# Kernel tuning notes

Hardware: AMD Instinct MI355X
Metric: run time of the kernel (lower is better)

## Reference

```python
import jax, jax.numpy as jnp
import numpy as np

DIM = 768
HEADS = 12
HD = DIM // HEADS
B, NX, NY = 8, 1024, 1024
GRID = 32
FREQ = 100.0
MLP_HID = 4 * DIM
EPS = 1e-5


def _grid_pos(batch, n, grid):
    g = int(np.sqrt(n))
    yy, xx = jnp.meshgrid(jnp.arange(g, dtype=jnp.int32), jnp.arange(g, dtype=jnp.int32), indexing='ij')
    pos = jnp.stack([yy.reshape(-1), xx.reshape(-1)], axis=-1)  # [N,2]
    return jnp.broadcast_to(pos[None], (batch, n, 2))


def setup_inputs() -> dict:
    key = jax.random.key(0)
    ks = jax.random.split(key, 16)
    s = 0.02
    inp = {
        'x': jax.random.normal(ks[0], (B, NX, DIM), jnp.float32),
        'y': jax.random.normal(ks[1], (B, NY, DIM), jnp.float32),
        'xpos': _grid_pos(B, NX, GRID),
        'ypos': _grid_pos(B, NY, GRID),
        # norms (gamma, beta)
        'norm1_g': jnp.ones((DIM,), jnp.float32), 'norm1_b': jnp.zeros((DIM,), jnp.float32),
        'norm2_g': jnp.ones((DIM,), jnp.float32), 'norm2_b': jnp.zeros((DIM,), jnp.float32),
        'norm3_g': jnp.ones((DIM,), jnp.float32), 'norm3_b': jnp.zeros((DIM,), jnp.float32),
        'normy_g': jnp.ones((DIM,), jnp.float32), 'normy_b': jnp.zeros((DIM,), jnp.float32),
        # self-attn: fused qkv (no bias, qkv_bias=False), out proj (with bias)
        'qkv_w': jax.random.normal(ks[2], (DIM, 3 * DIM), jnp.float32) * s,
        'attn_proj_w': jax.random.normal(ks[3], (DIM, DIM), jnp.float32) * s,
        'attn_proj_b': jnp.zeros((DIM,), jnp.float32),
        # cross-attn: separate q/k/v (no bias), out proj (with bias)
        'projq_w': jax.random.normal(ks[4], (DIM, DIM), jnp.float32) * s,
        'projk_w': jax.random.normal(ks[5], (DIM, DIM), jnp.float32) * s,
        'projv_w': jax.random.normal(ks[6], (DIM, DIM), jnp.float32) * s,
        'cross_proj_w': jax.random.normal(ks[7], (DIM, DIM), jnp.float32) * s,
        'cross_proj_b': jnp.zeros((DIM,), jnp.float32),
        # MLP
        'fc1_w': jax.random.normal(ks[8], (DIM, MLP_HID), jnp.float32) * s,
        'fc1_b': jnp.zeros((MLP_HID,), jnp.float32),
        'fc2_w': jax.random.normal(ks[9], (MLP_HID, DIM), jnp.float32) * s,
        'fc2_b': jnp.zeros((DIM,), jnp.float32),
    }
    return inp


def layernorm(x, g, b):
    m = jnp.mean(x, axis=-1, keepdims=True)
    v = jnp.mean(jnp.square(x - m), axis=-1, keepdims=True)
    return (x - m) * jax.lax.rsqrt(v + EPS) * g + b


def rope1d(tok, pos):
    # tok: [B,H,N,D], pos: [B,N] int
    D = tok.shape[-1]
    inv = 1.0 / (FREQ ** (jnp.arange(0, D, 2, dtype=jnp.float32) / D))  # [D/2]
    f = pos[:, None, :, None].astype(jnp.float32) * inv  # [B,1,N,D/2]
    emb = jnp.concatenate([f, f], axis=-1)  # [B,1,N,D]
    cos, sin = jnp.cos(emb), jnp.sin(emb)
    t1, t2 = jnp.split(tok, 2, axis=-1)
    rot = jnp.concatenate([-t2, t1], axis=-1)
    return tok * cos + rot * sin


def rope2d(tok, pos):
    # first half of head dim rotated by y-coord, second half by x-coord
    ty, tx = jnp.split(tok, 2, axis=-1)
    return jnp.concatenate([rope1d(ty, pos[..., 0]), rope1d(tx, pos[..., 1])], axis=-1)


def sdpa(q, k, v):
    scale = q.shape[-1] ** -0.5
    a = jax.nn.softmax(jnp.einsum('bhqd,bhkd->bhqk', q, k) * scale, axis=-1)
    return jnp.einsum('bhqk,bhkd->bhqd', a, v)


def split_heads(t):  # [B,N,C] -> [B,H,N,HD]
    Bv, N, C = t.shape
    return t.reshape(Bv, N, HEADS, HD).transpose(0, 2, 1, 3)


def merge_heads(t):  # [B,H,N,HD] -> [B,N,C]
    Bv, H, N, D = t.shape
    return t.transpose(0, 2, 1, 3).reshape(Bv, N, H * D)


def reference(x, y, xpos, ypos,
              norm1_g, norm1_b, norm2_g, norm2_b, norm3_g, norm3_b, normy_g, normy_b,
              qkv_w, attn_proj_w, attn_proj_b,
              projq_w, projk_w, projv_w, cross_proj_w, cross_proj_b,
              fc1_w, fc1_b, fc2_w, fc2_b):
    # --- self attention ---
    h = layernorm(x, norm1_g, norm1_b)
    qkv = h @ qkv_w  # [B,N,3C]
    q, k, v = (split_heads(t) for t in jnp.split(qkv, 3, axis=-1))
    q = rope2d(q, xpos)
    k = rope2d(k, xpos)
    x = x + merge_heads(sdpa(q, k, v)) @ attn_proj_w + attn_proj_b

    # --- cross attention ---
    y_ = layernorm(y, normy_g, normy_b)
    hq = layernorm(x, norm2_g, norm2_b)
    q = rope2d(split_heads(hq @ projq_w), xpos)
    k = rope2d(split_heads(y_ @ projk_w), ypos)
    v = split_heads(y_ @ projv_w)
    x = x + merge_heads(sdpa(q, k, v)) @ cross_proj_w + cross_proj_b

    # --- MLP ---
    h = layernorm(x, norm3_g, norm3_b)
    x = x + jax.nn.gelu(h @ fc1_w + fc1_b, approximate=False) @ fc2_w + fc2_b
    return (x, y)
```

## Files before the change

kernel.cpp:

```cpp
#include <hip/hip_runtime.h>
#include <hip/hip_bf16.h>
#include <math.h>

#define DIM 768
#define HEADS 12
#define HD 64
#define BB 8
#define NN 1024
#define EPSV 1e-5f

typedef unsigned int uint32;
typedef unsigned short ushort_t;
using short8 = __attribute__((ext_vector_type(8))) short;
using f32x4 = __attribute__((ext_vector_type(4))) float;

static __device__ inline ushort_t f2b(float v) {
    uint32 u = __float_as_uint(v);
    return (ushort_t)((u + 0x7FFFu + ((u >> 16) & 1u)) >> 16);
}
static __device__ inline float b2f(ushort_t v) {
    return __uint_as_float((uint32)v << 16);
}

static __device__ inline float erf_fast(float x) {
    float ax = fabsf(x);
    float t = __frcp_rn(1.0f + 0.3275911f * ax);
    float p = t * (0.254829592f + t * (-0.284496736f + t * (1.421413741f +
              t * (-1.453152027f + t * 1.061405429f))));
    float e = 1.0f - p * __expf(-ax * ax);
    return copysignf(e, x);
}

static __device__ __forceinline__ void gload_lds16(const ushort_t* g, ushort_t* l) {
    __builtin_amdgcn_global_load_lds(
        (const __attribute__((address_space(1))) void*)g,
        (__attribute__((address_space(3))) void*)l, 16, 0, 0);
}

__global__ __launch_bounds__(256) void ln_bf16(const float* __restrict__ in,
                                               const float* __restrict__ g,
                                               const float* __restrict__ b,
                                               ushort_t* __restrict__ out) {
    int r = blockIdx.x;
    const float* x = in + (size_t)r * DIM;
    ushort_t* o = out + (size_t)r * DIM;
    int t = threadIdx.x;
    float v0 = x[t], v1 = x[t + 256], v2 = x[t + 512];
    float s = v0 + v1 + v2;
    float s2 = v0 * v0 + v1 * v1 + v2 * v2;
    for (int off = 32; off; off >>= 1) {
        s += __shfl_xor(s, off);
        s2 += __shfl_xor(s2, off);
    }
    __shared__ float ls[4], lq[4];
    int wid = t >> 6;
    if ((t & 63) == 0) { ls[wid] = s; lq[wid] = s2; }
    __syncthreads();
    s = ls[0] + ls[1] + ls[2] + ls[3];
    s2 = lq[0] + lq[1] + lq[2] + lq[3];
    float mean = s * (1.0f / DIM);
    float var = s2 * (1.0f / DIM) - mean * mean;
    float rs = rsqrtf(var + EPSV);
    o[t]       = f2b((v0 - mean) * rs * g[t]       + b[t]);
    o[t + 256] = f2b((v1 - mean) * rs * g[t + 256] + b[t + 256]);
    o[t + 512] = f2b((v2 - mean) * rs * g[t + 512] + b[t + 512]);
}

struct XArgs {
    const float* src[8];
    ushort_t* dst[8];
    int K[8], N[8];
    int tstart[9];
};
__global__ __launch_bounds__(256) void xform_w(XArgs a) {
    __shared__ float tl[32][33];
    int t = blockIdx.x;
    int w = 0;
    while (t >= a.tstart[w + 1]) w++;
    int lt = t - a.tstart[w];
    int ntn = a.N[w] >> 5;
    int k0 = (lt / ntn) * 32, n0 = (lt % ntn) * 32;
    const float* src = a.src[w];
    ushort_t* dst = a.dst[w];
    int K = a.K[w], N = a.N[w];
    int rr = threadIdx.x >> 5, cc = threadIdx.x & 31;
#pragma unroll
    for (int u = 0; u < 4; u++)
        tl[rr + u * 8][cc] = src[(size_t)(k0 + rr + u * 8) * N + n0 + cc];
    __syncthreads();
#pragma unroll
    for (int u = 0; u < 4; u++)
        dst[(size_t)(n0 + rr + u * 8) * K + k0 + cc] = f2b(tl[cc][rr + u * 8]);
}

template <int ACT, int OBF16>
__global__ __launch_bounds__(256) void gemm_mfma(const ushort_t* __restrict__ A,
                                                 const ushort_t* __restrict__ Wt,
                                                 const float* __restrict__ bias,
                                                 const float* res,
                                                 void* Cout, int M, int N, int K) {
    __shared__ ushort_t lds[4][128 * 32];
    int bid = blockIdx.x;
    int xcd = bid & 7, rr = bid >> 3;
    int bx = rr >> 3;
    int by = xcd * 8 + (rr & 7);
    int m0 = by * 128, n0 = bx * 128;
    int tid = threadIdx.x;
    int wid = tid >> 6, lane = tid & 63;
    int wm = wid >> 1, wn = wid & 1;
    int l15 = lane & 15, lh = lane >> 4;

    int srow = lane >> 2, cslot = lane & 3;

    auto STAGE = [&](int buf, int k0) {
#pragma unroll
        for (int inst = 0; inst < 2; inst++) {
            int r0 = (wid * 2 + inst) * 16 + srow;
            int swzr = (r0 & 3) ^ ((r0 >> 2) & 3);
            int csrc = (cslot ^ swzr) << 3;
            gload_lds16(A + (size_t)(m0 + r0) * K + k0 + csrc,
                        &lds[buf * 2 + 0][(wid * 2 + inst) * 512]);
            gload_lds16(Wt + (size_t)(n0 + r0) * K + k0 + csrc,
                        &lds[buf * 2 + 1][(wid * 2 + inst) * 512]);
        }
    };

    STAGE(0, 0);
    f32x4 acc[4][4] = {};
    __syncthreads();

    int nT = K >> 5;
    int cur = 0;
    for (int t = 0; t < nT; t++) {
        if (t + 1 < nT) STAGE(cur ^ 1, (t + 1) << 5);
        short8 af[4], bfr[4];
#pragma unroll
        for (int i = 0; i < 4; i++) {
            int rA = wm * 64 + i * 16 + l15;
            int sA = lh ^ ((rA & 3) ^ ((rA >> 2) & 3));
            af[i] = *(const short8*)&lds[cur * 2 + 0][rA * 32 + (sA << 3)];
            int rB = wn * 64 + i * 16 + l15;
            int sB = lh ^ ((rB & 3) ^ ((rB >> 2) & 3));
            bfr[i] = *(const short8*)&lds[cur * 2 + 1][rB * 32 + (sB << 3)];
        }
#pragma unroll
        for (int i = 0; i < 4; i++)
#pragma unroll
            for (int j = 0; j < 4; j++)
                acc[i][j] = __builtin_amdgcn_mfma_f32_16x16x32_bf16(
                    af[i], bfr[j], acc[i][j], 0, 0, 0);
        __syncthreads();
        cur ^= 1;
    }

    float* ep = (float*)&lds[0][0] + wid * 1088;
    int erow = lane >> 2, ecol = (lane & 3) * 16;
#pragma unroll
    for (int i = 0; i < 4; i++) {
#pragma unroll
        for (int j = 0; j < 4; j++) {
            int n = n0 + wn * 64 + j * 16 + l15;
            float bv = bias ? bias[n] : 0.0f;
#pragma unroll
            for (int r = 0; r < 4; r++) {
                float v = acc[i][j][r] + bv;
                if (ACT == 1) v = 0.5f * v * (1.0f + erf_fast(v * 0.70710678118654752f));
                ep[(lh * 4 + r) * 68 + j * 16 + l15] = v;
            }
        }
        int m = m0 + wm * 64 + i * 16 + erow;
        size_t off = (size_t)m * N + n0 + wn * 64 + ecol;
        float vv[16];
#pragma unroll
        for (int u = 0; u < 4; u++)
            *(float4*)&vv[u * 4] = *(float4*)&ep[erow * 68 + ecol + u * 4];
        if (res) {
#pragma unroll
            for (int u = 0; u < 4; u++) {
                float4 rv = *(const float4*)(res + off + u * 4);
                vv[u * 4 + 0] += rv.x;
                vv[u * 4 + 1] += rv.y;
                vv[u * 4 + 2] += rv.z;
                vv[u * 4 + 3] += rv.w;
            }
        }
        if (OBF16) {
            ushort_t tb[16];
#pragma unroll
            for (int u = 0; u < 16; u++) tb[u] = f2b(vv[u]);
            *(uint4*)((ushort_t*)Cout + off)     = *(uint4*)&tb[0];
            *(uint4*)((ushort_t*)Cout + off + 8) = *(uint4*)&tb[8];
        } else {
#pragma unroll
            for (int u = 0; u < 4; u++)
                *(float4*)((float*)Cout + off + u * 4) = *(float4*)&vv[u * 4];
        }
    }
}

__global__ __launch_bounds__(256) void rope2_bf16(ushort_t* __restrict__ ta,
                                                  const int* __restrict__ pa, int sa,
                                                  ushort_t* __restrict__ tb,
                                                  const int* __restrict__ pb, int sb,
                                                  int rt) {
    int idx = blockIdx.x * 256 + threadIdx.x;
    ushort_t* t;
    const int* pos;
    int rowStride;
    if (idx >= rt) { idx -= rt; t = tb; pos = pb; rowStride = sb; }
    else           { t = ta; pos = pa; rowStride = sa; }
    int i = idx & 15;
    int half = (idx >> 4) & 1;
    int h = (idx >> 5) % HEADS;
    int bn = idx / (HEADS * 32);
    int p = pos[(size_t)bn * 2 + half];
    float inv = powf(100.0f, -(float)i / 16.0f);
    float f = (float)p * inv;
    float c, s;
    sincosf(f, &s, &c);
    ushort_t* base = t + (size_t)bn * rowStride + h * HD + half * 32;
    float t1 = b2f(base[i]), t2 = b2f(base[i + 16]);
    base[i]      = f2b(t1 * c - t2 * s);
    base[i + 16] = f2b(t2 * c + t1 * s);
}

__global__ __launch_bounds__(256) void transpose_v(const ushort_t* __restrict__ src,
                                                   int ss, ushort_t* __restrict__ dst) {
    __shared__ ushort_t tl[64][66];
    int bid = blockIdx.x;
    int nt = bid & 15;
    int h = (bid >> 4) % HEADS;
    int b = bid / (16 * HEADS);
    int n0 = nt * 64;
    int t = threadIdx.x;
    int r = t >> 2, c0 = (t & 3) * 16;
    const ushort_t* s = src + ((size_t)(b * NN) + n0 + r) * ss + h * HD + c0;
    *(uint4*)&tl[r][c0]     = *(const uint4*)s;
    *(uint4*)&tl[r][c0 + 8] = *(const uint4*)(s + 8);
    __syncthreads();
    ushort_t* d = dst + (((size_t)(b * HEADS + h)) * HD + r) * NN + n0 + c0;
    ushort_t tmp[16];
#pragma unroll
    for (int u = 0; u < 16; u++) tmp[u] = tl[c0 + u][r];
    *(uint4*)d       = *(uint4*)tmp;
    *(uint4*)(d + 8) = *(uint4*)(tmp + 8);
}

__global__ __launch_bounds__(256) void attn_mfma(const ushort_t* __restrict__ Q, int sq,
                                                 const ushort_t* __restrict__ K, int sk,
                                                 const ushort_t* __restrict__ VT,
                                                 ushort_t* __restrict__ O, int so) {
    __shared__ ushort_t Qs[64][72];
    __shared__ ushort_t Ks[64][72];
    __shared__ ushort_t Vs[64][72];
    __shared__ ushort_t Ps[64][72];

    int g = blockIdx.x;
    int bid = (g & 7) * 192 + (g >> 3);
    int qb = bid & 15;
    int h = (bid >> 4) % HEADS;
    int b = bid / (16 * HEADS);
    int n0 = qb * 64;

    int tid = threadIdx.x;
    int lane = tid & 63, wq = tid >> 6;
    int l15 = lane & 15, lh = lane >> 4;

    const ushort_t* Qbase = Q + (size_t)b * NN * sq + h * HD;
    const ushort_t* Kbase = K + (size_t)b * NN * sk + h * HD;
    const ushort_t* VTbase = VT + ((size_t)(b * HEADS + h)) * HD * NN;
    ushort_t* Obase = O + (size_t)b * NN * so + h * HD;

    int row = tid >> 2, c0 = (tid & 3) * 16;
    {
        const ushort_t* src = Qbase + (size_t)(n0 + row) * sq + c0;
        *(uint4*)&Qs[row][c0]     = *(const uint4*)src;
        *(uint4*)&Qs[row][c0 + 8] = *(const uint4*)(src + 8);
    }

    const ushort_t* kp = Kbase + (size_t)row * sk + c0;
    const ushort_t* vp = VTbase + (size_t)row * NN + c0;
    uint4 rk0 = *(const uint4*)kp, rk1 = *(const uint4*)(kp + 8);
    uint4 rv0 = *(const uint4*)vp, rv1 = *(const uint4*)(vp + 8);

    f32x4 oacc[4] = {};
    float mrow[4] = {-1e30f, -1e30f, -1e30f, -1e30f};
    float lrow[4] = {};

    for (int kt = 0; kt < NN / 64; kt++) {
        __syncthreads();
        *(uint4*)&Ks[row][c0]     = rk0;
        *(uint4*)&Ks[row][c0 + 8] = rk1;
        *(uint4*)&Vs[row][c0]     = rv0;
        *(uint4*)&Vs[row][c0 + 8] = rv1;
        __syncthreads();
        if (kt + 1 < NN / 64) {
            const ushort_t* kp2 = kp + (size_t)(kt + 1) * 64 * sk;
            const ushort_t* vp2 = vp + (size_t)(kt + 1) * 64;
            rk0 = *(const uint4*)kp2;
            rk1 = *(const uint4*)(kp2 + 8);
            rv0 = *(const uint4*)vp2;
            rv1 = *(const uint4*)(vp2 + 8);
        }

        f32x4 s[4] = {};
#pragma unroll
        for (int ks8 = 0; ks8 < 2; ks8++) {
            short8 aq = *(const short8*)&Qs[wq * 16 + l15][ks8 * 32 + lh * 8];
#pragma unroll
            for (int j = 0; j < 4; j++) {
                short8 bk = *(const short8*)&Ks[j * 16 + l15][ks8 * 32 + lh * 8];
                s[j] = __builtin_amdgcn_mfma_f32_16x16x32_bf16(aq, bk, s[j], 0, 0, 0);
            }
        }

        float corr[4];
#pragma unroll
        for (int r = 0; r < 4; r++) {
            float v0 = s[0][r] * 0.125f, v1 = s[1][r] * 0.125f;
            float v2 = s[2][r] * 0.125f, v3 = s[3][r] * 0.125f;
            float rm = fmaxf(fmaxf(v0, v1), fmaxf(v2, v3));
            rm = fmaxf(rm, __shfl_xor(rm, 1));
            rm = fmaxf(rm, __shfl_xor(rm, 2));
            rm = fmaxf(rm, __shfl_xor(rm, 4));
            rm = fmaxf(rm, __shfl_xor(rm, 8));
            float mn = fmaxf(mrow[r], rm);
            corr[r] = __expf(mrow[r] - mn);
            mrow[r] = mn;
            float p0 = __expf(v0 - mn), p1 = __expf(v1 - mn);
            float p2 = __expf(v2 - mn), p3 = __expf(v3 - mn);
            float ps = p0 + p1 + p2 + p3;
            ps += __shfl_xor(ps, 1);
            ps += __shfl_xor(ps, 2);
            ps += __shfl_xor(ps, 4);
            ps += __shfl_xor(ps, 8);
            lrow[r] = lrow[r] * corr[r] + ps;
            int qrow = wq * 16 + lh * 4 + r;
            Ps[qrow][0 * 16 + l15] = f2b(p0);
            Ps[qrow][1 * 16 + l15] = f2b(p1);
            Ps[qrow][2 * 16 + l15] = f2b(p2);
            Ps[qrow][3 * 16 + l15] = f2b(p3);
        }
#pragma unroll
        for (int j = 0; j < 4; j++)
#pragma unroll
            for (int r = 0; r < 4; r++) oacc[j][r] *= corr[r];

#pragma unroll
        for (int ks8 = 0; ks8 < 2; ks8++) {
            short8 ap = *(const short8*)&Ps[wq * 16 + l15][ks8 * 32 + lh * 8];
#pragma unroll
            for (int j = 0; j < 4; j++) {
                short8 bv = *(const short8*)&Vs[j * 16 + l15][ks8 * 32 + lh * 8];
                oacc[j] = __builtin_amdgcn_mfma_f32_16x16x32_bf16(ap, bv, oacc[j], 0, 0, 0);
            }
        }
    }

#pragma unroll
    for (int r = 0; r < 4; r++) {
        float inv = 1.0f / lrow[r];
        int prow = wq * 16 + lh * 4 + r;
#pragma unroll
        for (int j = 0; j < 4; j++)
            Ps[prow][j * 16 + l15] = f2b(oacc[j][r] * inv);
    }
    int erow = lane >> 2, ecol = (lane & 3) * 16;
    uint4 w0 = *(uint4*)&Ps[wq * 16 + erow][ecol];
    uint4 w1 = *(uint4*)&Ps[wq * 16 + erow][ecol + 8];
    ushort_t* op = Obase + (size_t)(n0 + wq * 16 + erow) * so + ecol;
    *(uint4*)op       = w0;
    *(uint4*)(op + 8) = w1;
}

__global__ __launch_bounds__(256) void fill_f32(float* __restrict__ out, float v, int n) {
    int i = blockIdx.x * 256 + threadIdx.x;
    if (i < n) out[i] = v;
}

extern "C" void kernel_launch(void* const* d_in, const int* in_sizes, int n_in,
                              void* d_out, int out_size, void* d_ws, size_t ws_size,
                              hipStream_t stream) {
    const float* x = (const float*)d_in[0];
    const float* y = (const float*)d_in[1];
    const int* xpos = (const int*)d_in[2];
    const int* ypos = (const int*)d_in[3];
    const float* norm1_g = (const float*)d_in[4];
    const float* norm1_b = (const float*)d_in[5];
    const float* norm2_g = (const float*)d_in[6];
    const float* norm2_b = (const float*)d_in[7];
    const float* norm3_g = (const float*)d_in[8];
    const float* norm3_b = (const float*)d_in[9];
    const float* normy_g = (const float*)d_in[10];
    const float* normy_b = (const float*)d_in[11];
    const float* qkv_w = (const float*)d_in[12];
    const float* attn_proj_w = (const float*)d_in[13];
    const float* attn_proj_b = (const float*)d_in[14];
    const float* projq_w = (const float*)d_in[15];
    const float* projk_w = (const float*)d_in[16];
    const float* projv_w = (const float*)d_in[17];
    const float* cross_proj_w = (const float*)d_in[18];
    const float* cross_proj_b = (const float*)d_in[19];
    const float* fc1_w = (const float*)d_in[20];
    const float* fc1_b = (const float*)d_in[21];
    const float* fc2_w = (const float*)d_in[22];
    const float* fc2_b = (const float*)d_in[23];
    float* out = (float*)d_out;

    const size_t SZ = (size_t)BB * NN * DIM;
    const int ROWS = BB * NN;

    const size_t WS_NEED = SZ * 4 + SZ * 2 + 4 * SZ * 2 + 9437184ull * 2;

    {
        const int expect[24] = {
            (int)SZ, (int)SZ, BB * NN * 2, BB * NN * 2,
            DIM, DIM, DIM, DIM, DIM, DIM, DIM, DIM,
            DIM * 3 * DIM, DIM * DIM, DIM,
            DIM * DIM, DIM * DIM, DIM * DIM, DIM * DIM, DIM,
            DIM * 4 * DIM, 4 * DIM, 4 * DIM * DIM, DIM};
        float sentinel = 0.0f;
        if (n_in != 24) sentinel = 2000.0f;
        else {
            for (int i = 0; i < 24; i++)
                if (in_sizes[i] != expect[i]) { sentinel = 1000.0f + i; break; }
        }
        if (sentinel == 0.0f && ws_size < WS_NEED) sentinel = 3000.0f;
        if (sentinel == 0.0f && out_size != (int)(2 * SZ)) sentinel = 4000.0f;
        if (sentinel != 0.0f) {
            fill_f32<<<(int)((SZ + 255) / 256), 256, 0, stream>>>(out, sentinel, (int)SZ);
            return;
        }
    }

    float* bufX = (float*)d_ws;
    ushort_t* bufAb = (ushort_t*)(bufX + SZ);
    ushort_t* bufQKVb = bufAb + SZ;
    ushort_t* wts = bufQKVb + 4 * SZ;

    ushort_t* qkvT = wts;
    ushort_t* apT  = qkvT + 2304 * 768;
    ushort_t* pqT  = apT + 768 * 768;
    ushort_t* pkT  = pqT + 768 * 768;
    ushort_t* pvT  = pkT + 768 * 768;
    ushort_t* cpT  = pvT + 768 * 768;
    ushort_t* fc1T = cpT + 768 * 768;
    ushort_t* fc2T = fc1T + 3072 * 768;
    ushort_t* HID  = bufQKVb;

    XArgs xa;
    xa.src[0] = qkv_w;        xa.dst[0] = qkvT; xa.K[0] = 768;  xa.N[0] = 2304;
    xa.src[1] = attn_proj_w;  xa.dst[1] = apT;  xa.K[1] = 768;  xa.N[1] = 768;
    xa.src[2] = projq_w;      xa.dst[2] = pqT;  xa.K[2] = 768;  xa.N[2] = 768;
    xa.src[3] = projk_w;      xa.dst[3] = pkT;  xa.K[3] = 768;  xa.N[3] = 768;
    xa.src[4] = projv_w;      xa.dst[4] = pvT;  xa.K[4] = 768;  xa.N[4] = 768;
    xa.src[5] = cross_proj_w; xa.dst[5] = cpT;  xa.K[5] = 768;  xa.N[5] = 768;
    xa.src[6] = fc1_w;        xa.dst[6] = fc1T; xa.K[6] = 768;  xa.N[6] = 3072;
    xa.src[7] = fc2_w;        xa.dst[7] = fc2T; xa.K[7] = 3072; xa.N[7] = 768;
    int acc_t = 0;
    for (int i = 0; i < 8; i++) {
        xa.tstart[i] = acc_t;
        acc_t += (xa.K[i] / 32) * (xa.N[i] / 32);
    }
    xa.tstart[8] = acc_t;
    xform_w<<<acc_t, 256, 0, stream>>>(xa);

    const int rt = ROWS * HEADS * 32;
    const int attnGrid = BB * HEADS * (NN / 64);
    ushort_t* VTg;

    ln_bf16<<<ROWS, 256, 0, stream>>>(x, norm1_g, norm1_b, bufAb);
    gemm_mfma<0, 1><<<64 * 18, 256, 0, stream>>>(bufAb, qkvT, nullptr, nullptr,
                                                 bufQKVb, ROWS, 2304, 768);
    rope2_bf16<<<2 * rt / 256, 256, 0, stream>>>(bufQKVb, xpos, 2304,
                                                 bufQKVb + DIM, xpos, 2304, rt);
    VTg = bufQKVb + 3 * SZ;
    transpose_v<<<attnGrid, 256, 0, stream>>>(bufQKVb + 2 * DIM, 2304, VTg);
    attn_mfma<<<attnGrid, 256, 0, stream>>>(bufQKVb, 2304, bufQKVb + DIM, 2304,
                                            VTg, bufAb, DIM);
    gemm_mfma<0, 0><<<64 * 6, 256, 0, stream>>>(bufAb, apT, attn_proj_b, x,
                                                bufX, ROWS, 768, 768);

    ushort_t* Qc = bufQKVb;
    ushort_t* KVc = bufQKVb + SZ;
    ln_bf16<<<ROWS, 256, 0, stream>>>(bufX, norm2_g, norm2_b, bufAb);
    gemm_mfma<0, 1><<<64 * 6, 256, 0, stream>>>(bufAb, pqT, nullptr, nullptr,
                                                Qc, ROWS, 768, 768);
    ln_bf16<<<ROWS, 256, 0, stream>>>(y, normy_g, normy_b, bufAb);
    gemm_mfma<0, 1><<<64 * 12, 256, 0, stream>>>(bufAb, pkT, nullptr, nullptr,
                                                 KVc, ROWS, 1536, 768);
    rope2_bf16<<<2 * rt / 256, 256, 0, stream>>>(Qc, xpos, 768,
                                                 KVc, ypos, 1536, rt);
    VTg = bufQKVb + 3 * SZ;
    transpose_v<<<attnGrid, 256, 0, stream>>>(KVc + DIM, 1536, VTg);
    attn_mfma<<<attnGrid, 256, 0, stream>>>(Qc, 768, KVc, 1536, VTg, bufAb, DIM);
    gemm_mfma<0, 0><<<64 * 6, 256, 0, stream>>>(bufAb, cpT, cross_proj_b, bufX,
                                                bufX, ROWS, 768, 768);

    ln_bf16<<<ROWS, 256, 0, stream>>>(bufX, norm3_g, norm3_b, bufAb);
    gemm_mfma<1, 1><<<64 * 24, 256, 0, stream>>>(bufAb, fc1T, fc1_b, nullptr,
                                                 HID, ROWS, 3072, 768);
    gemm_mfma<0, 0><<<64 * 6, 256, 0, stream>>>(HID, fc2T, fc2_b, bufX,
                                                out, ROWS, 768, 3072);

    hipMemcpyAsync(out + SZ, y, SZ * sizeof(float), hipMemcpyDeviceToDevice, stream);
}
```

Baseline: 555.7 us.

## Fold softmax scale and log2e into Q, use exp2 with lazy max rescaling

Pre-multiplies Q by scale*log2(e) as it is loaded into shared memory, so the softmax can use exp2f directly without per-score multiplies. It also adds a lazy rescale: the running max and the output accumulator are only corrected when some row's new max exceeds the old one by a threshold, checked wave-uniformly. The aim is to cut exp and multiply work in the attention inner loop. The cost is an extra bf16 rounding of the scaled Q, and probabilities that may exceed 1 (bounded by the threshold) before normalisation.

```diff
diff --git a/kernel.cpp b/kernel.cpp
--- a/kernel.cpp
+++ b/kernel.cpp
@@ -271,11 +271,22 @@
     const ushort_t* VTbase = VT + ((size_t)(b * HEADS + h)) * HD * NN;
     ushort_t* Obase = O + (size_t)b * NN * so + h * HD;
 
+    const float SCL = 0.18033688011112042f;
     int row = tid >> 2, c0 = (tid & 3) * 16;
     {
         const ushort_t* src = Qbase + (size_t)(n0 + row) * sq + c0;
-        *(uint4*)&Qs[row][c0]     = *(const uint4*)src;
-        *(uint4*)&Qs[row][c0 + 8] = *(const uint4*)(src + 8);
+        uint4 q0 = *(const uint4*)src;
+        uint4 q1 = *(const uint4*)(src + 8);
+        ushort_t* qp0 = (ushort_t*)&q0;
+        ushort_t* qp1 = (ushort_t*)&q1;
+        ushort_t t0[8], t1[8];
+#pragma unroll
+        for (int u = 0; u < 8; u++) {
+            t0[u] = f2b(b2f(qp0[u]) * SCL);
+            t1[u] = f2b(b2f(qp1[u]) * SCL);
+        }
+        *(uint4*)&Qs[row][c0]     = *(uint4*)t0;
+        *(uint4*)&Qs[row][c0 + 8] = *(uint4*)t1;
     }
 
     const ushort_t* kp = Kbase + (size_t)row * sk + c0;
@@ -314,37 +325,52 @@
             }
         }
 
-        float corr[4];
+        float rm4[4];
+        bool ok = true;
 #pragma unroll
         for (int r = 0; r < 4; r++) {
-            float v0 = s[0][r] * 0.125f, v1 = s[1][r] * 0.125f;
-            float v2 = s[2][r] * 0.125f, v3 = s[3][r] * 0.125f;
-            float rm = fmaxf(fmaxf(v0, v1), fmaxf(v2, v3));
+            float rm = fmaxf(fmaxf(s[0][r], s[1][r]), fmaxf(s[2][r], s[3][r]));
             rm = fmaxf(rm, __shfl_xor(rm, 1));
             rm = fmaxf(rm, __shfl_xor(rm, 2));
             rm = fmaxf(rm, __shfl_xor(rm, 4));
             rm = fmaxf(rm, __shfl_xor(rm, 8));
-            float mn = fmaxf(mrow[r], rm);
-            corr[r] = __expf(mrow[r] - mn);
-            mrow[r] = mn;
-            float p0 = __expf(v0 - mn), p1 = __expf(v1 - mn);
-            float p2 = __expf(v2 - mn), p3 = __expf(v3 - mn);
+            rm4[r] = rm;
+            ok = ok && (rm <= mrow[r] + 11.5417f);
+        }
+        bool need = !__all(ok);
+
+        float corr[4];
+        if (need) {
+#pragma unroll
+            for (int r = 0; r < 4; r++) {
+                float mn = fmaxf(mrow[r], rm4[r]);
+                corr[r] = exp2f(mrow[r] - mn);
+                mrow[r] = mn;
+            }
+        }
+#pragma unroll
+        for (int r = 0; r < 4; r++) {
+            float mn = mrow[r];
+            float p0 = exp2f(s[0][r] - mn), p1 = exp2f(s[1][r] - mn);
+            float p2 = exp2f(s[2][r] - mn), p3 = exp2f(s[3][r] - mn);
             float ps = p0 + p1 + p2 + p3;
             ps += __shfl_xor(ps, 1);
             ps += __shfl_xor(ps, 2);
             ps += __shfl_xor(ps, 4);
             ps += __shfl_xor(ps, 8);
-            lrow[r] = lrow[r] * corr[r] + ps;
+            lrow[r] = need ? lrow[r] * corr[r] + ps : lrow[r] + ps;
             int qrow = wq * 16 + lh * 4 + r;
             Ps[qrow][0 * 16 + l15] = f2b(p0);
             Ps[qrow][1 * 16 + l15] = f2b(p1);
             Ps[qrow][2 * 16 + l15] = f2b(p2);
             Ps[qrow][3 * 16 + l15] = f2b(p3);
         }
-#pragma unroll
-        for (int j = 0; j < 4; j++)
-#pragma unroll
-            for (int r = 0; r < 4; r++) oacc[j][r] *= corr[r];
+        if (need) {
+#pragma unroll
+            for (int j = 0; j < 4; j++)
+#pragma unroll
+                for (int r = 0; r < 4; r++) oacc[j][r] *= corr[r];
+        }
 
 #pragma unroll
         for (int ks8 = 0; ks8 < 2; ks8++) {
```

Result: slower. 578.5 us (+4.1%).
